# Kernel tuning notes

Measured on AMD Instinct MI355X. Metric: run time of the kernel, lower is better.

Reference implementation:

```python
import jax, jax.numpy as jnp
import numpy as np

N_NODES = 100000


def gcn_conv(x, edge_index, W, b):
    """PyG GCNConv: h = x @ W; out = D^-1/2 (A+I) D^-1/2 h + b."""
    n = x.shape[0]
    src, dst = edge_index[0], edge_index[1]
    loop = jnp.arange(n)
    src = jnp.concatenate([src, loop])  # add self-loops
    dst = jnp.concatenate([dst, loop])
    # degree at target nodes (unit edge weights)
    deg = jax.ops.segment_sum(jnp.ones(dst.shape[0], dtype=x.dtype), dst, num_segments=n)
    dinv = jnp.where(deg > 0, jax.lax.rsqrt(deg), 0.0)
    norm = dinv[src] * dinv[dst]  # [E+n]
    h = x @ W  # [n, out]
    msg = h[src] * norm[:, None]  # gather + scale
    out = jax.ops.segment_sum(msg, dst, num_segments=n)  # scatter-add
    return out + b


def setup_inputs() -> dict:
    key = jax.random.key(0)
    k1, k2, k3, k4, k5, k6 = jax.random.split(key, 6)
    E = 3200000
    x = jax.random.normal(k1, (N_NODES, 2), dtype=jnp.float32)
    edge_index = jax.random.randint(k2, (2, E), 0, N_NODES, dtype=jnp.int64)
    W1 = jax.random.normal(k3, (2, 16), dtype=jnp.float32) * 0.5
    b1 = jax.random.normal(k4, (16,), dtype=jnp.float32) * 0.1
    W2 = jax.random.normal(k5, (16, 2), dtype=jnp.float32) * 0.25
    b2 = jax.random.normal(k6, (2,), dtype=jnp.float32) * 0.1
    return {"x": x, "edge_index": edge_index, "W1": W1, "b1": b1, "W2": W2, "b2": b2}


def reference(x, edge_index, W1, b1, W2, b2):
    h = jax.nn.relu(gcn_conv(x, edge_index, W1, b1))
    # dropout is identity at inference
    out = gcn_conv(h, edge_index, W2, b2)
    return jax.nn.log_softmax(out, axis=1)
```

## Files before the change

### kernel.cpp

```cpp
#include <hip/hip_runtime.h>
#include <math.h>


constexpr int N = 100000;
constexpr int LOGB = 6;
constexpr int BNODES = 1 << LOGB;
constexpr int K = (N + BNODES - 1) / BNODES;
constexpr int KF = 49 * 32;
constexpr int CAPF = 2560;
constexpr int NC = 49;
constexpr int CAP1 = 68608;
constexpr int BSP = 512;
constexpr int ECHUNK = 8192;
constexpr int EPT = ECHUNK / BSP;
constexpr int MAXCH = 9;

__global__ __launch_bounds__(BSP) void k_pass1(const int* __restrict__ src,
                                               const int* __restrict__ dst, int E,
                                               int* __restrict__ gfill1,
                                               int* __restrict__ slotsC) {
    __shared__ int hist[NC];
    __shared__ int base[NC];
    int t = threadIdx.x;
    if (t < NC) hist[t] = 0;
    __syncthreads();
    int s[EPT], d[EPT];
    int ebase = blockIdx.x * ECHUNK + t * EPT;
#pragma unroll
    for (int k = 0; k < EPT / 4; k++) {
        int idx = ebase + 4 * k;
        if (idx + 3 < E) {
            *(int4*)(s + 4 * k) = *(const int4*)(src + idx);
            *(int4*)(d + 4 * k) = *(const int4*)(dst + idx);
        } else {
            for (int j = 0; j < 4; j++) {
                s[4 * k + j] = (idx + j < E) ? src[idx + j] : -1;
                d[4 * k + j] = (idx + j < E) ? dst[idx + j] : -1;
            }
        }
    }
#pragma unroll
    for (int k = 0; k < EPT; k++)
        if (d[k] >= 0) atomicAdd(&hist[d[k] >> 11], 1);
    __syncthreads();
    if (t < NC) {
        int c = hist[t];
        base[t] = c ? atomicAdd(&gfill1[t], c) : 0;
        hist[t] = 0;
    }
    __syncthreads();
#pragma unroll
    for (int k = 0; k < EPT; k++) {
        if (d[k] >= 0) {
            int bin = d[k] >> 11;
            int r = atomicAdd(&hist[bin], 1);
            int pos = base[bin] + r;
            if (pos < CAP1) slotsC[bin * CAP1 + pos] = (s[k] << 11) | (d[k] & 2047);
        }
    }
}

__global__ __launch_bounds__(BSP) void k_pass2(const int* __restrict__ gfill1,
                                               const int* __restrict__ slotsC,
                                               int* __restrict__ gfillF,
                                               int* __restrict__ slotsF,
                                               int* __restrict__ cntp) {
    __shared__ int hist[32];
    __shared__ int base[32];
    __shared__ int cnt[2048];
    int c = blockIdx.x / MAXCH;
    int j = blockIdx.x % MAXCH;
    int t = threadIdx.x;
    if (t < 32) hist[t] = 0;
    for (int i = t; i < 2048; i += BSP) cnt[i] = 0;
    __syncthreads();
    int fill = min(gfill1[c], CAP1);
    int e0 = j * ECHUNK;
    int e1 = min(fill, e0 + ECHUNK);
    const int* row = slotsC + c * CAP1;
    int v[EPT];
    int ebase = e0 + t * EPT;
#pragma unroll
    for (int k = 0; k < EPT / 4; k++) {
        int idx = ebase + 4 * k;
        if (idx + 3 < e1) {
            *(int4*)(v + 4 * k) = *(const int4*)(row + idx);
        } else {
            for (int jj = 0; jj < 4; jj++) v[4 * k + jj] = (idx + jj < e1) ? row[idx + jj] : -1;
        }
    }
#pragma unroll
    for (int k = 0; k < EPT; k++) {
        if (v[k] >= 0) {
            atomicAdd(&hist[(v[k] >> 6) & 31], 1);
            atomicAdd(&cnt[v[k] & 2047], 1);
        }
    }
    __syncthreads();
    if (t < 32) {
        int cc = hist[t];
        base[t] = cc ? atomicAdd(&gfillF[c * 32 + t], cc) : 0;
        hist[t] = 0;
    }
    __syncthreads();
#pragma unroll
    for (int k = 0; k < EPT; k++) {
        if (v[k] >= 0) {
            int b = (v[k] >> 6) & 31;
            int r = atomicAdd(&hist[b], 1);
            int pos = base[b] + r;
            if (pos < CAPF)
                slotsF[(c * 32 + b) * CAPF + pos] = ((v[k] >> 11) << 6) | (v[k] & 63);
        }
    }
    int* out = cntp + (size_t)blockIdx.x * 2048;
    *(int4*)(out + 4 * t) = *(const int4*)(cnt + 4 * t);
}

__global__ void k_node1(const int* __restrict__ cntp, const float* __restrict__ x,
                        float* __restrict__ dinv, float2* __restrict__ sx) {
    int i = blockIdx.x * blockDim.x + threadIdx.x;
    if (i >= N) return;
    int c = i >> 11, l = i & 2047;
    const int* p = cntp + (size_t)c * MAXCH * 2048 + l;
    int s = 0;
#pragma unroll
    for (int j = 0; j < MAXCH; j++) s += p[j * 2048];
    float di = rsqrtf((float)(s + 1));
    dinv[i] = di;
    float2 xv = ((const float2*)x)[i];
    sx[i] = make_float2(xv.x * di, xv.y * di);
}

__device__ __forceinline__ int4 gload(const int* __restrict__ row, int j, int cnt) {
    if (j + 3 < cnt) return *(const int4*)(row + j);
    int4 p = make_int4(-1, -1, -1, -1);
    if (j + 0 < cnt) p.x = row[j + 0];
    if (j + 1 < cnt) p.y = row[j + 1];
    if (j + 2 < cnt) p.z = row[j + 2];
    if (j + 3 < cnt) p.w = row[j + 3];
    return p;
}

__global__ __launch_bounds__(256) void k_agg1(const int* __restrict__ gfillF,
                                              const int* __restrict__ slotsF,
                                              const float* __restrict__ dinv,
                                              const float2* __restrict__ sx,
                                              const float* __restrict__ W1,
                                              const float* __restrict__ b1,
                                              const float* __restrict__ W2,
                                              float2* __restrict__ sz) {
    __shared__ float accX[BNODES], accY[BNODES];
    __shared__ float sW1[32], sb1[16], sW2[32];
    int t = threadIdx.x;
    if (t < 32) sW1[t] = W1[t];
    if (t >= 32 && t < 48) sb1[t - 32] = b1[t - 32];
    if (t >= 48 && t < 80) sW2[t - 48] = W2[t - 48];
    if (t < BNODES) { accX[t] = 0.f; accY[t] = 0.f; }
    __syncthreads();
    int b = blockIdx.x;
    int count = min(gfillF[b], CAPF);
    const int* row = slotsF + (size_t)b * CAPF;
    int pk[12];
    {
        int4 p0 = gload(row, 4 * t, count);
        int4 p1 = gload(row, 4 * t + 1024, count);
        int4 p2 = gload(row, 4 * t + 2048, count);
        pk[0] = p0.x; pk[1] = p0.y; pk[2] = p0.z; pk[3] = p0.w;
        pk[4] = p1.x; pk[5] = p1.y; pk[6] = p1.z; pk[7] = p1.w;
        pk[8] = p2.x; pk[9] = p2.y; pk[10] = p2.z; pk[11] = p2.w;
    }
    float2 vv[12];
#pragma unroll
    for (int m = 0; m < 12; m++) {
        int idx = (pk[m] >= 0) ? (pk[m] >> LOGB) : 0;
        vv[m] = sx[idx];
    }
#pragma unroll
    for (int m = 0; m < 12; m++) {
        if (pk[m] >= 0) {
            atomicAdd(&accX[pk[m] & (BNODES - 1)], vv[m].x);
            atomicAdd(&accY[pk[m] & (BNODES - 1)], vv[m].y);
        }
    }
    __syncthreads();
    if (t < BNODES) {
        int node = b * BNODES + t;
        if (node < N) {
            float di = dinv[node];
            float2 sv = sx[node];
            float a0 = (accX[t] + sv.x) * di;
            float a1 = (accY[t] + sv.y) * di;
            float z0 = 0.f, z1 = 0.f;
#pragma unroll
            for (int k = 0; k < 16; k++) {
                float h = fmaf(a0, sW1[k], fmaf(a1, sW1[16 + k], sb1[k]));
                h = fmaxf(h, 0.f);
                z0 = fmaf(h, sW2[2 * k + 0], z0);
                z1 = fmaf(h, sW2[2 * k + 1], z1);
            }
            sz[node] = make_float2(z0 * di, z1 * di);
        }
    }
}

__global__ __launch_bounds__(256) void k_agg2(const int* __restrict__ gfillF,
                                              const int* __restrict__ slotsF,
                                              const float* __restrict__ dinv,
                                              const float2* __restrict__ sz,
                                              const float* __restrict__ b2,
                                              float2* __restrict__ out) {
    __shared__ float accX[BNODES], accY[BNODES];
    int b = blockIdx.x, t = threadIdx.x;
    if (t < BNODES) { accX[t] = 0.f; accY[t] = 0.f; }
    __syncthreads();
    int count = min(gfillF[b], CAPF);
    const int* row = slotsF + (size_t)b * CAPF;
    int pk[12];
    {
        int4 p0 = gload(row, 4 * t, count);
        int4 p1 = gload(row, 4 * t + 1024, count);
        int4 p2 = gload(row, 4 * t + 2048, count);
        pk[0] = p0.x; pk[1] = p0.y; pk[2] = p0.z; pk[3] = p0.w;
        pk[4] = p1.x; pk[5] = p1.y; pk[6] = p1.z; pk[7] = p1.w;
        pk[8] = p2.x; pk[9] = p2.y; pk[10] = p2.z; pk[11] = p2.w;
    }
    float2 vv[12];
#pragma unroll
    for (int m = 0; m < 12; m++) {
        int idx = (pk[m] >= 0) ? (pk[m] >> LOGB) : 0;
        vv[m] = sz[idx];
    }
#pragma unroll
    for (int m = 0; m < 12; m++) {
        if (pk[m] >= 0) {
            atomicAdd(&accX[pk[m] & (BNODES - 1)], vv[m].x);
            atomicAdd(&accY[pk[m] & (BNODES - 1)], vv[m].y);
        }
    }
    __syncthreads();
    if (t < BNODES) {
        int node = b * BNODES + t;
        if (node < N) {
            float di = dinv[node];
            float2 sv = sz[node];
            float v0 = fmaf(accX[t] + sv.x, di, b2[0]);
            float v1 = fmaf(accY[t] + sv.y, di, b2[1]);
            float m = fmaxf(v0, v1);
            float lse = m + logf(expf(v0 - m) + expf(v1 - m));
            out[node] = make_float2(v0 - lse, v1 - lse);
        }
    }
}

extern "C" void kernel_launch(void* const* d_in, const int* in_sizes, int n_in,
                              void* d_out, int out_size, void* d_ws, size_t ws_size,
                              hipStream_t stream) {
    const float* x  = (const float*)d_in[0];
    const int*   ei = (const int*)d_in[1];
    const float* W1 = (const float*)d_in[2];
    const float* b1 = (const float*)d_in[3];
    const float* W2 = (const float*)d_in[4];
    const float* b2 = (const float*)d_in[5];

    const int E = in_sizes[1] / 2;
    const int* src = ei;
    const int* dst = ei + E;
    const int GP = (E + ECHUNK - 1) / ECHUNK;

    char* ws = (char*)d_ws;
    size_t off = 0;
    auto alloc = [&](size_t bytes) {
        char* p = ws + off;
        off += (bytes + 511) & ~size_t(511);
        return p;
    };
    int*    fills  = (int*)alloc((NC + KF) * sizeof(int));
    float*  dinv   = (float*)alloc(N * sizeof(float));
    float2* sx     = (float2*)alloc(N * sizeof(float2));
    float2* sz     = (float2*)alloc(N * sizeof(float2));
    int*    slotsC = (int*)alloc((size_t)NC * CAP1 * sizeof(int));
    int*    slotsF = (int*)alloc((size_t)KF * CAPF * sizeof(int));
    int*    cntp   = (int*)alloc((size_t)NC * MAXCH * 2048 * sizeof(int));
    int* gfill1 = fills;
    int* gfillF = fills + NC;

    hipMemsetAsync(fills, 0, (NC + KF) * sizeof(int), stream);

    k_pass1<<<GP, BSP, 0, stream>>>(src, dst, E, gfill1, slotsC);
    k_pass2<<<NC * MAXCH, BSP, 0, stream>>>(gfill1, slotsC, gfillF, slotsF, cntp);
    k_node1<<<(N + 255) / 256, 256, 0, stream>>>(cntp, x, dinv, sx);
    k_agg1<<<K, 256, 0, stream>>>(gfillF, slotsF, dinv, sx, W1, b1, W2, sz);
    k_agg2<<<K, 256, 0, stream>>>(gfillF, slotsF, dinv, sz, b2, (float2*)d_out);
}
```

Measured before the change: 203.5 us.

## Bucket edges into 2D src/dst tiles and aggregate from shared-memory source slices

Edges are now bucketed by (dst chunk, src chunk) tile instead of by fine dst block. Each tile block stages its 2048 source values in LDS, so the gather becomes a shared-memory read rather than a random global read. Partial sums per tile are written to a global buffer and reduced over the 49 source chunks in separate reduce kernels. This swaps random global gathers for extra partial-sum traffic (about 2401x2048 float2 per layer) and two additional kernel launches. It also adds a per-tile capacity limit (1700) that could overflow on skewed inputs.

```diff
diff --git a/kernel.cpp b/kernel.cpp
--- a/kernel.cpp
+++ b/kernel.cpp
@@ -3,13 +3,12 @@
 
 
 constexpr int N = 100000;
-constexpr int LOGB = 6;
-constexpr int BNODES = 1 << LOGB;
-constexpr int K = (N + BNODES - 1) / BNODES;
-constexpr int KF = 49 * 32;
-constexpr int CAPF = 2560;
+constexpr int CLOG = 11;
+constexpr int CN = 1 << CLOG;
 constexpr int NC = 49;
+constexpr int TIL = NC * NC;
 constexpr int CAP1 = 68608;
+constexpr int CAPT = 1700;
 constexpr int BSP = 512;
 constexpr int ECHUNK = 8192;
 constexpr int EPT = ECHUNK / BSP;
@@ -41,7 +40,7 @@
     }
 #pragma unroll
     for (int k = 0; k < EPT; k++)
-        if (d[k] >= 0) atomicAdd(&hist[d[k] >> 11], 1);
+        if (d[k] >= 0) atomicAdd(&hist[d[k] >> CLOG], 1);
     __syncthreads();
     if (t < NC) {
         int c = hist[t];
@@ -52,27 +51,27 @@
 #pragma unroll
     for (int k = 0; k < EPT; k++) {
         if (d[k] >= 0) {
-            int bin = d[k] >> 11;
+            int bin = d[k] >> CLOG;
             int r = atomicAdd(&hist[bin], 1);
             int pos = base[bin] + r;
-            if (pos < CAP1) slotsC[bin * CAP1 + pos] = (s[k] << 11) | (d[k] & 2047);
+            if (pos < CAP1) slotsC[bin * CAP1 + pos] = (s[k] << CLOG) | (d[k] & (CN - 1));
         }
     }
 }
 
 __global__ __launch_bounds__(BSP) void k_pass2(const int* __restrict__ gfill1,
                                                const int* __restrict__ slotsC,
-                                               int* __restrict__ gfillF,
-                                               int* __restrict__ slotsF,
+                                               int* __restrict__ gfillT,
+                                               int* __restrict__ slotsT,
                                                int* __restrict__ cntp) {
-    __shared__ int hist[32];
-    __shared__ int base[32];
-    __shared__ int cnt[2048];
+    __shared__ int hist[NC];
+    __shared__ int base[NC];
+    __shared__ int cnt[CN];
     int c = blockIdx.x / MAXCH;
     int j = blockIdx.x % MAXCH;
     int t = threadIdx.x;
-    if (t < 32) hist[t] = 0;
-    for (int i = t; i < 2048; i += BSP) cnt[i] = 0;
+    if (t < NC) hist[t] = 0;
+    for (int i = t; i < CN; i += BSP) cnt[i] = 0;
     __syncthreads();
     int fill = min(gfill1[c], CAP1);
     int e0 = j * ECHUNK;
@@ -92,28 +91,30 @@
 #pragma unroll
     for (int k = 0; k < EPT; k++) {
         if (v[k] >= 0) {
-            atomicAdd(&hist[(v[k] >> 6) & 31], 1);
-            atomicAdd(&cnt[v[k] & 2047], 1);
-        }
-    }
-    __syncthreads();
-    if (t < 32) {
+            atomicAdd(&hist[v[k] >> (2 * CLOG)], 1);
+            atomicAdd(&cnt[v[k] & (CN - 1)], 1);
+        }
+    }
+    __syncthreads();
+    if (t < NC) {
         int cc = hist[t];
-        base[t] = cc ? atomicAdd(&gfillF[c * 32 + t], cc) : 0;
+        base[t] = cc ? atomicAdd(&gfillT[c * NC + t], cc) : 0;
         hist[t] = 0;
     }
     __syncthreads();
 #pragma unroll
     for (int k = 0; k < EPT; k++) {
         if (v[k] >= 0) {
-            int b = (v[k] >> 6) & 31;
-            int r = atomicAdd(&hist[b], 1);
-            int pos = base[b] + r;
-            if (pos < CAPF)
-                slotsF[(c * 32 + b) * CAPF + pos] = ((v[k] >> 11) << 6) | (v[k] & 63);
-        }
-    }
-    int* out = cntp + (size_t)blockIdx.x * 2048;
+            int sb = v[k] >> (2 * CLOG);
+            int r = atomicAdd(&hist[sb], 1);
+            int pos = base[sb] + r;
+            if (pos < CAPT) {
+                int f = (((v[k] >> CLOG) & (CN - 1)) << CLOG) | (v[k] & (CN - 1));
+                slotsT[(c * NC + sb) * CAPT + pos] = f;
+            }
+        }
+    }
+    int* out = cntp + (size_t)blockIdx.x * CN;
     *(int4*)(out + 4 * t) = *(const int4*)(cnt + 4 * t);
 }
 
@@ -121,11 +122,11 @@
                         float* __restrict__ dinv, float2* __restrict__ sx) {
     int i = blockIdx.x * blockDim.x + threadIdx.x;
     if (i >= N) return;
-    int c = i >> 11, l = i & 2047;
-    const int* p = cntp + (size_t)c * MAXCH * 2048 + l;
+    int c = i >> CLOG, l = i & (CN - 1);
+    const int* p = cntp + (size_t)c * MAXCH * CN + l;
     int s = 0;
 #pragma unroll
-    for (int j = 0; j < MAXCH; j++) s += p[j * 2048];
+    for (int j = 0; j < MAXCH; j++) s += p[j * CN];
     float di = rsqrtf((float)(s + 1));
     dinv[i] = di;
     float2 xv = ((const float2*)x)[i];
@@ -142,115 +143,94 @@
     return p;
 }
 
-__global__ __launch_bounds__(256) void k_agg1(const int* __restrict__ gfillF,
-                                              const int* __restrict__ slotsF,
-                                              const float* __restrict__ dinv,
-                                              const float2* __restrict__ sx,
-                                              const float* __restrict__ W1,
-                                              const float* __restrict__ b1,
-                                              const float* __restrict__ W2,
-                                              float2* __restrict__ sz) {
-    __shared__ float accX[BNODES], accY[BNODES];
+__global__ __launch_bounds__(BSP) void k_tile(const int* __restrict__ gfillT,
+                                              const int* __restrict__ slotsT,
+                                              const float2* __restrict__ val,
+                                              float2* __restrict__ P) {
+    __shared__ float2 sv[CN];
+    __shared__ float2 acc[CN];
+    int T = blockIdx.x;
+    int sb = T % NC;
+    int t = threadIdx.x;
+#pragma unroll
+    for (int k = 0; k < CN / BSP; k++) {
+        int idx = t + k * BSP;
+        int node = (sb << CLOG) + idx;
+        sv[idx] = (node < N) ? val[node] : make_float2(0.f, 0.f);
+        acc[idx] = make_float2(0.f, 0.f);
+    }
+    __syncthreads();
+    int count = min(gfillT[T], CAPT);
+    const int* row = slotsT + (size_t)T * CAPT;
+    int4 p = gload(row, 4 * t, count);
+    if (p.x >= 0) { float2 v = sv[p.x >> CLOG]; atomicAdd(&acc[p.x & (CN - 1)].x, v.x); atomicAdd(&acc[p.x & (CN - 1)].y, v.y); }
+    if (p.y >= 0) { float2 v = sv[p.y >> CLOG]; atomicAdd(&acc[p.y & (CN - 1)].x, v.x); atomicAdd(&acc[p.y & (CN - 1)].y, v.y); }
+    if (p.z >= 0) { float2 v = sv[p.z >> CLOG]; atomicAdd(&acc[p.z & (CN - 1)].x, v.x); atomicAdd(&acc[p.z & (CN - 1)].y, v.y); }
+    if (p.w >= 0) { float2 v = sv[p.w >> CLOG]; atomicAdd(&acc[p.w & (CN - 1)].x, v.x); atomicAdd(&acc[p.w & (CN - 1)].y, v.y); }
+    __syncthreads();
+    float4* dst4 = (float4*)(P + (size_t)T * CN);
+    const float4* acc4 = (const float4*)acc;
+#pragma unroll
+    for (int k = 0; k < CN / (2 * BSP); k++) dst4[t + k * BSP] = acc4[t + k * BSP];
+}
+
+__global__ void k_reduce1(const float2* __restrict__ P, const float* __restrict__ dinv,
+                          const float2* __restrict__ sx, const float* __restrict__ W1,
+                          const float* __restrict__ b1, const float* __restrict__ W2,
+                          float2* __restrict__ sz) {
     __shared__ float sW1[32], sb1[16], sW2[32];
     int t = threadIdx.x;
     if (t < 32) sW1[t] = W1[t];
     if (t >= 32 && t < 48) sb1[t - 32] = b1[t - 32];
     if (t >= 48 && t < 80) sW2[t - 48] = W2[t - 48];
-    if (t < BNODES) { accX[t] = 0.f; accY[t] = 0.f; }
-    __syncthreads();
-    int b = blockIdx.x;
-    int count = min(gfillF[b], CAPF);
-    const int* row = slotsF + (size_t)b * CAPF;
-    int pk[12];
-    {
-        int4 p0 = gload(row, 4 * t, count);
-        int4 p1 = gload(row, 4 * t + 1024, count);
-        int4 p2 = gload(row, 4 * t + 2048, count);
-        pk[0] = p0.x; pk[1] = p0.y; pk[2] = p0.z; pk[3] = p0.w;
-        pk[4] = p1.x; pk[5] = p1.y; pk[6] = p1.z; pk[7] = p1.w;
-        pk[8] = p2.x; pk[9] = p2.y; pk[10] = p2.z; pk[11] = p2.w;
-    }
-    float2 vv[12];
-#pragma unroll
-    for (int m = 0; m < 12; m++) {
-        int idx = (pk[m] >= 0) ? (pk[m] >> LOGB) : 0;
-        vv[m] = sx[idx];
-    }
-#pragma unroll
-    for (int m = 0; m < 12; m++) {
-        if (pk[m] >= 0) {
-            atomicAdd(&accX[pk[m] & (BNODES - 1)], vv[m].x);
-            atomicAdd(&accY[pk[m] & (BNODES - 1)], vv[m].y);
-        }
-    }
-    __syncthreads();
-    if (t < BNODES) {
-        int node = b * BNODES + t;
-        if (node < N) {
-            float di = dinv[node];
-            float2 sv = sx[node];
-            float a0 = (accX[t] + sv.x) * di;
-            float a1 = (accY[t] + sv.y) * di;
-            float z0 = 0.f, z1 = 0.f;
-#pragma unroll
-            for (int k = 0; k < 16; k++) {
-                float h = fmaf(a0, sW1[k], fmaf(a1, sW1[16 + k], sb1[k]));
-                h = fmaxf(h, 0.f);
-                z0 = fmaf(h, sW2[2 * k + 0], z0);
-                z1 = fmaf(h, sW2[2 * k + 1], z1);
-            }
-            sz[node] = make_float2(z0 * di, z1 * di);
-        }
-    }
-}
-
-__global__ __launch_bounds__(256) void k_agg2(const int* __restrict__ gfillF,
-                                              const int* __restrict__ slotsF,
-                                              const float* __restrict__ dinv,
-                                              const float2* __restrict__ sz,
-                                              const float* __restrict__ b2,
-                                              float2* __restrict__ out) {
-    __shared__ float accX[BNODES], accY[BNODES];
-    int b = blockIdx.x, t = threadIdx.x;
-    if (t < BNODES) { accX[t] = 0.f; accY[t] = 0.f; }
-    __syncthreads();
-    int count = min(gfillF[b], CAPF);
-    const int* row = slotsF + (size_t)b * CAPF;
-    int pk[12];
-    {
-        int4 p0 = gload(row, 4 * t, count);
-        int4 p1 = gload(row, 4 * t + 1024, count);
-        int4 p2 = gload(row, 4 * t + 2048, count);
-        pk[0] = p0.x; pk[1] = p0.y; pk[2] = p0.z; pk[3] = p0.w;
-        pk[4] = p1.x; pk[5] = p1.y; pk[6] = p1.z; pk[7] = p1.w;
-        pk[8] = p2.x; pk[9] = p2.y; pk[10] = p2.z; pk[11] = p2.w;
-    }
-    float2 vv[12];
-#pragma unroll
-    for (int m = 0; m < 12; m++) {
-        int idx = (pk[m] >= 0) ? (pk[m] >> LOGB) : 0;
-        vv[m] = sz[idx];
-    }
-#pragma unroll
-    for (int m = 0; m < 12; m++) {
-        if (pk[m] >= 0) {
-            atomicAdd(&accX[pk[m] & (BNODES - 1)], vv[m].x);
-            atomicAdd(&accY[pk[m] & (BNODES - 1)], vv[m].y);
-        }
-    }
-    __syncthreads();
-    if (t < BNODES) {
-        int node = b * BNODES + t;
-        if (node < N) {
-            float di = dinv[node];
-            float2 sv = sz[node];
-            float v0 = fmaf(accX[t] + sv.x, di, b2[0]);
-            float v1 = fmaf(accY[t] + sv.y, di, b2[1]);
-            float m = fmaxf(v0, v1);
-            float lse = m + logf(expf(v0 - m) + expf(v1 - m));
-            out[node] = make_float2(v0 - lse, v1 - lse);
-        }
-    }
+    __syncthreads();
+    int i = blockIdx.x * blockDim.x + t;
+    if (i >= N) return;
+    int c = i >> CLOG, nl = i & (CN - 1);
+    const float2* p = P + (size_t)(c * NC) * CN + nl;
+    float a0 = 0.f, a1 = 0.f;
+#pragma unroll 7
+    for (int k = 0; k < NC; k++) {
+        float2 v = p[(size_t)k * CN];
+        a0 += v.x;
+        a1 += v.y;
+    }
+    float di = dinv[i];
+    float2 sv = sx[i];
+    a0 = (a0 + sv.x) * di;
+    a1 = (a1 + sv.y) * di;
+    float z0 = 0.f, z1 = 0.f;
+#pragma unroll
+    for (int k = 0; k < 16; k++) {
+        float h = fmaf(a0, sW1[k], fmaf(a1, sW1[16 + k], sb1[k]));
+        h = fmaxf(h, 0.f);
+        z0 = fmaf(h, sW2[2 * k + 0], z0);
+        z1 = fmaf(h, sW2[2 * k + 1], z1);
+    }
+    sz[i] = make_float2(z0 * di, z1 * di);
+}
+
+__global__ void k_reduce2(const float2* __restrict__ P, const float* __restrict__ dinv,
+                          const float2* __restrict__ sz, const float* __restrict__ b2,
+                          float2* __restrict__ out) {
+    int i = blockIdx.x * blockDim.x + threadIdx.x;
+    if (i >= N) return;
+    int c = i >> CLOG, nl = i & (CN - 1);
+    const float2* p = P + (size_t)(c * NC) * CN + nl;
+    float a0 = 0.f, a1 = 0.f;
+#pragma unroll 7
+    for (int k = 0; k < NC; k++) {
+        float2 v = p[(size_t)k * CN];
+        a0 += v.x;
+        a1 += v.y;
+    }
+    float di = dinv[i];
+    float2 sv = sz[i];
+    float v0 = fmaf(a0 + sv.x, di, b2[0]);
+    float v1 = fmaf(a1 + sv.y, di, b2[1]);
+    float m = fmaxf(v0, v1);
+    float lse = m + logf(expf(v0 - m) + expf(v1 - m));
+    out[i] = make_float2(v0 - lse, v1 - lse);
 }
 
 extern "C" void kernel_launch(void* const* d_in, const int* in_sizes, int n_in,
@@ -275,21 +255,24 @@
         off += (bytes + 511) & ~size_t(511);
         return p;
     };
-    int*    fills  = (int*)alloc((NC + KF) * sizeof(int));
+    int*    fills  = (int*)alloc((NC + TIL) * sizeof(int));
     float*  dinv   = (float*)alloc(N * sizeof(float));
     float2* sx     = (float2*)alloc(N * sizeof(float2));
     float2* sz     = (float2*)alloc(N * sizeof(float2));
     int*    slotsC = (int*)alloc((size_t)NC * CAP1 * sizeof(int));
-    int*    slotsF = (int*)alloc((size_t)KF * CAPF * sizeof(int));
-    int*    cntp   = (int*)alloc((size_t)NC * MAXCH * 2048 * sizeof(int));
+    int*    slotsT = (int*)alloc((size_t)TIL * CAPT * sizeof(int));
+    int*    cntp   = (int*)alloc((size_t)NC * MAXCH * CN * sizeof(int));
+    float2* P      = (float2*)alloc((size_t)TIL * CN * sizeof(float2));
     int* gfill1 = fills;
-    int* gfillF = fills + NC;
-
-    hipMemsetAsync(fills, 0, (NC + KF) * sizeof(int), stream);
+    int* gfillT = fills + NC;
+
+    hipMemsetAsync(fills, 0, (NC + TIL) * sizeof(int), stream);
 
     k_pass1<<<GP, BSP, 0, stream>>>(src, dst, E, gfill1, slotsC);
-    k_pass2<<<NC * MAXCH, BSP, 0, stream>>>(gfill1, slotsC, gfillF, slotsF, cntp);
+    k_pass2<<<NC * MAXCH, BSP, 0, stream>>>(gfill1, slotsC, gfillT, slotsT, cntp);
     k_node1<<<(N + 255) / 256, 256, 0, stream>>>(cntp, x, dinv, sx);
-    k_agg1<<<K, 256, 0, stream>>>(gfillF, slotsF, dinv, sx, W1, b1, W2, sz);
-    k_agg2<<<K, 256, 0, stream>>>(gfillF, slotsF, dinv, sz, b2, (float2*)d_out);
-}
+    k_tile<<<TIL, BSP, 0, stream>>>(gfillT, slotsT, sx, P);
+    k_reduce1<<<(N + 255) / 256, 256, 0, stream>>>(P, dinv, sx, W1, b1, W2, sz);
+    k_tile<<<TIL, BSP, 0, stream>>>(gfillT, slotsT, sz, P);
+    k_reduce2<<<(N + 255) / 256, 256, 0, stream>>>(P, dinv, sz, b2, (float2*)d_out);
+}
```

Result: slower. 221.0 us (+8.6%).
